# Kernel tuning notes

Hardware: AMD Instinct MI355X
Metric: run time of the kernel (lower is better)

Reference implementation:

```python
import jax, jax.numpy as jnp
import numpy as np

B, S, D, H = 4, 1024, 1024, 16
HD = D // H


def setup_inputs() -> dict:
    key = jax.random.key(0)
    ks = jax.random.split(key, 12)
    s = 1.0 / np.sqrt(D)
    inp = {
        'q': jax.random.normal(ks[0], (B, S, D), jnp.float32),
        'k': jax.random.normal(ks[1], (B, S, D), jnp.float32),
        'v': jax.random.normal(ks[2], (B, S, D), jnp.float32),
        'mask': jnp.broadcast_to(jnp.tril(jnp.ones((S, S), jnp.int32)), (B, S, S)),
        'Wq': jax.random.uniform(ks[3], (D, D), jnp.float32, -s, s),
        'bq': jax.random.uniform(ks[4], (D,), jnp.float32, -s, s),
        'Wk': jax.random.uniform(ks[5], (D, D), jnp.float32, -s, s),
        'bk': jax.random.uniform(ks[6], (D,), jnp.float32, -s, s),
        'Wv': jax.random.uniform(ks[7], (D, D), jnp.float32, -s, s),
        'bv': jax.random.uniform(ks[8], (D,), jnp.float32, -s, s),
        'Wo': jax.random.uniform(ks[9], (D, D), jnp.float32, -s, s),
        'bo': jax.random.uniform(ks[10], (D,), jnp.float32, -s, s),
    }
    return inp


def _split_heads(x):
    # [B,S,D] -> [B,H,S,HD]
    b, s, d = x.shape
    return x.reshape(b, s, H, HD).transpose(0, 2, 1, 3)


def reference(q, k, v, mask, Wq, bq, Wk, bk, Wv, bv, Wo, bo):
    # Linear projections (torch Linear: x @ W.T + b) followed by relu
    qh = jax.nn.relu(q @ Wq.T + bq)
    kh = jax.nn.relu(k @ Wk.T + bk)
    vh = jax.nn.relu(v @ Wv.T + bv)
    qh, kh, vh = _split_heads(qh), _split_heads(kh), _split_heads(vh)
    scores = jnp.einsum('bhqd,bhkd->bhqk', qh, kh) / jnp.sqrt(jnp.float32(HD))
    scores = jnp.where(mask[:, None, :, :] == 0, jnp.float32(-1e9), scores)
    attn = jax.nn.softmax(scores, axis=-1)
    y = jnp.einsum('bhqk,bhkd->bhqd', attn, vh)
    y = y.transpose(0, 2, 1, 3).reshape(B, S, D)  # merge heads
    return jax.nn.relu(y @ Wo.T + bo)
```

## Files before the change

### kernel.cpp

```cpp
#include <hip/hip_runtime.h>


using f16    = _Float16;
using f16x4  = __attribute__((ext_vector_type(4))) _Float16;
using f16x8  = __attribute__((ext_vector_type(8))) _Float16;
using f32x4  = __attribute__((ext_vector_type(4))) float;
using f32x16 = __attribute__((ext_vector_type(16))) float;

static constexpr int S = 1024, Dm = 1024, NH = 16, HD = 64;

#if __has_builtin(__builtin_amdgcn_mfma_f32_32x32x16_f16)
#define USE_G32 1
#define MFMA32(ACC, A_, B_) \
    (ACC) = __builtin_amdgcn_mfma_f32_32x32x16_f16((A_), (B_), (ACC), 0, 0, 0)
#else
#define USE_G32 0
#endif

#if __has_builtin(__builtin_amdgcn_mfma_f32_16x16x32_f16) && \
    __has_builtin(__builtin_amdgcn_mfma_f32_16x16x16f16)
#define USE_A16 1
#define MFMA16K32(ACC, A_, B_) \
    (ACC) = __builtin_amdgcn_mfma_f32_16x16x32_f16((A_), (B_), (ACC), 0, 0, 0)
#define MFMA16(ACC, A_, B_) \
    (ACC) = __builtin_amdgcn_mfma_f32_16x16x16f16((A_), (B_), (ACC), 0, 0, 0)
#else
#define USE_A16 0
#endif

#define LO4(v) __builtin_shufflevector((v), (v), 0, 1, 2, 3)
#define HI4(v) __builtin_shufflevector((v), (v), 4, 5, 6, 7)

__device__ __forceinline__ f16x4 cvt4(float4 a) {
    f16x4 r; r[0] = (f16)a.x; r[1] = (f16)a.y; r[2] = (f16)a.z; r[3] = (f16)a.w;
    return r;
}

__device__ __forceinline__ int pcol64(int k) {
#if USE_A16
    return ((k >> 3) & 3) * 16 + ((k >> 5) << 3) + (k & 7);
#else
    return ((k >> 2) & 3) * 16 + ((k >> 4) << 2) + (k & 3);
#endif
}

__device__ __forceinline__ int swz(int row, int col) {
    return (col & ~31) | ((((col >> 3) ^ (row >> 1)) & 3) << 3) | (col & 7);
}

__device__ __forceinline__ void store_out(void* out, int mode, int m, int n, float v) {
    if (mode == 2) {
        ((float*)out)[(size_t)m * Dm + n] = v;
    } else {
        const int b_ = m >> 10, s_ = m & 1023, h_ = n >> 6, hd_ = n & 63;
        const size_t idx = (mode == 0)
            ? (((size_t)(b_ * NH + h_) * S + s_) * HD + pcol64(hd_))
            : (((size_t)(b_ * NH + h_) * HD + hd_) * S + s_);
        ((f16*)out)[idx] = (f16)v;
    }
}

#if __has_builtin(__builtin_amdgcn_global_load_lds)
#define HAS_GLL 1
#else
#define HAS_GLL 0
#endif

__device__ __forceinline__ void gll16(const f16* g, f16* l) {
#if HAS_GLL
    __builtin_amdgcn_global_load_lds(
        (const __attribute__((address_space(1))) void*)g,
        (__attribute__((address_space(3))) void*)l, 16, 0, 0);
#else
    *(uint4*)l = *(const uint4*)g;
#endif
}

__global__ __launch_bounds__(256)
void cvt_w(const float* __restrict__ s0, const float* __restrict__ s1,
           const float* __restrict__ s2, f16* __restrict__ dst)
{
    const int z = blockIdx.y;
    const float* src = (z == 0) ? s0 : (z == 1) ? s1 : s2;
    const int e = blockIdx.x * 256 + threadIdx.x;
    const int n = e >> 8;
    const int k = (e & 255) * 4;
    const float4 v = *(const float4*)(src + (size_t)n * Dm + k);
    *(f16x4*)(dst + (size_t)z * Dm * Dm + (size_t)n * Dm + swz(n, k)) = cvt4(v);
}

template <int ADMA>
__device__ __forceinline__ void gemm_core(const void* __restrict__ A,
                                          const f16* __restrict__ Wf,
                                          const float* __restrict__ bias,
                                          void* __restrict__ out, int mode)
{
    const int tid = threadIdx.x;
    const int bm = blockIdx.x, bn = blockIdx.y;
#if USE_G32
    __shared__ alignas(16) f16 As[3][128][32];
    __shared__ alignas(16) f16 Ws[3][128][32];

    const int lane = tid & 63, wave = tid >> 6;
    const int l31 = lane & 31, kh = lane >> 5;
    const int wm = wave & 1, wn = wave >> 1;

    const int drow = wave * 16 + (lane >> 2);
    const int dcol = (lane & 3) * 8;
    const f16* Wsrc = Wf + (size_t)(bn * 128 + drow) * Dm + dcol;
    const f16* Asrc = (const f16*)A + (size_t)(bm * 128 + drow) * Dm + dcol;

    auto dma = [&](int k0, int buf) {
        gll16(Wsrc + k0, &Ws[buf][drow][dcol]);
        gll16(Wsrc + k0 + (size_t)64 * Dm, &Ws[buf][64 + drow][dcol]);
        if (ADMA) {
            gll16(Asrc + k0, &As[buf][drow][dcol]);
            gll16(Asrc + k0 + (size_t)64 * Dm, &As[buf][64 + drow][dcol]);
        }
    };

    const int ar = tid >> 1, ah = tid & 1;
    const float* Af = (const float*)A + (size_t)(bm * 128 + ar) * Dm + ah * 16;

    auto prefA = [&](int k0, float4 (&pa)[4]) {
#pragma unroll
        for (int j = 0; j < 4; ++j) pa[j] = *(const float4*)(Af + k0 + j * 4);
    };
    auto stageA = [&](int buf, const float4 (&pa)[4]) {
#pragma unroll
        for (int j2 = 0; j2 < 2; ++j2) {
            f16x8 v;
            const float4 a0 = pa[j2 * 2], a1 = pa[j2 * 2 + 1];
            v[0] = (f16)a0.x; v[1] = (f16)a0.y; v[2] = (f16)a0.z; v[3] = (f16)a0.w;
            v[4] = (f16)a1.x; v[5] = (f16)a1.y; v[6] = (f16)a1.z; v[7] = (f16)a1.w;
            const int phys = ((ah * 2 + j2) ^ ((ar >> 1) & 3)) & 3;
            *(f16x8*)&As[buf][ar][phys * 8] = v;
        }
    };

    f32x16 acc[2][2] = {};

    auto kslice = [&](int buf, int s) {
        const int sl = s * 2 + kh;
        const int rA0 = wm * 64 + l31,  rA1 = wm * 64 + 32 + l31;
        const int rB0 = wn * 64 + l31,  rB1 = wn * 64 + 32 + l31;
        const f16x8 af0 = *(const f16x8*)&As[buf][rA0][((sl ^ ((rA0 >> 1) & 3)) & 3) * 8];
        const f16x8 af1 = *(const f16x8*)&As[buf][rA1][((sl ^ ((rA1 >> 1) & 3)) & 3) * 8];
        const f16x8 bf0 = *(const f16x8*)&Ws[buf][rB0][((sl ^ ((rB0 >> 1) & 3)) & 3) * 8];
        const f16x8 bf1 = *(const f16x8*)&Ws[buf][rB1][((sl ^ ((rB1 >> 1) & 3)) & 3) * 8];
        MFMA32(acc[0][0], af0, bf0);
        MFMA32(acc[0][1], af0, bf1);
        MFMA32(acc[1][0], af1, bf0);
        MFMA32(acc[1][1], af1, bf1);
    };

    constexpr int NIT = Dm / 32;
    float4 paA[4], paB[4];

    if (!ADMA) prefA(0, paA);
    dma(0, 0);
    if (!ADMA) prefA(32, paB);
    dma(32, 1);
    if (!ADMA) stageA(0, paA);

    auto iter = [&](int t, float4 (&pnew)[4], const float4 (&pold)[4]) {
        if (t < NIT - 1) {
            if (ADMA) asm volatile("s_waitcnt vmcnt(4)" ::: "memory");
            else      asm volatile("s_waitcnt vmcnt(6)" ::: "memory");
        } else {
            asm volatile("s_waitcnt vmcnt(0)" ::: "memory");
        }
        asm volatile("s_waitcnt lgkmcnt(0)" ::: "memory");
        __builtin_amdgcn_s_barrier();
        __builtin_amdgcn_sched_barrier(0);
        const int cb = t % 3;
        if (t + 2 < NIT) {
            if (!ADMA) prefA((t + 2) * 32, pnew);
            dma((t + 2) * 32, (t + 2) % 3);
        }
        kslice(cb, 0);
        if (!ADMA && t + 1 < NIT) stageA((t + 1) % 3, pold);
        kslice(cb, 1);
    };

    for (int t = 0; t < NIT; t += 2) {
        iter(t, paA, paB);
        iter(t + 1, paB, paA);
    }

#pragma unroll
    for (int g2 = 0; g2 < 2; ++g2) {
        const int col = bn * 128 + wn * 64 + g2 * 32 + l31;
        const float bb = bias[col];
#pragma unroll
        for (int g = 0; g < 2; ++g)
#pragma unroll
            for (int blk = 0; blk < 4; ++blk) {
                const int row0 = bm * 128 + wm * 64 + g * 32 + 8 * blk + 4 * kh;
                if (mode == 1) {
                    const int b_ = row0 >> 10, s_ = row0 & 1023;
                    const int h_ = col >> 6, hd_ = col & 63;
                    f16x4 vv;
#pragma unroll
                    for (int r = 0; r < 4; ++r)
                        vv[r] = (f16)fmaxf(acc[g][g2][blk * 4 + r] + bb, 0.0f);
                    *(f16x4*)&((f16*)out)[((size_t)(b_ * NH + h_) * HD + hd_) * S + s_] = vv;
                } else {
#pragma unroll
                    for (int r = 0; r < 4; ++r)
                        store_out(out, mode, row0 + r, col,
                                  fmaxf(acc[g][g2][blk * 4 + r] + bb, 0.0f));
                }
            }
    }
#else
    for (int i = tid; i < 128 * 128; i += 256) {
        const int m = bm * 128 + (i >> 7);
        const int n = bn * 128 + (i & 127);
        float acc = 0.0f;
        for (int k2 = 0; k2 < Dm; ++k2) {
            const float a = ADMA ? (float)((const f16*)A)[(size_t)m * Dm + swz(m, k2)]
                                 : ((const float*)A)[(size_t)m * Dm + k2];
            acc = fmaf(a, (float)Wf[(size_t)n * Dm + swz(n, k2)], acc);
        }
        store_out(out, mode, m, n, fmaxf(acc + bias[n], 0.0f));
    }
#endif
}

__global__ __launch_bounds__(256, 3)
void gemm_qkv(const float* __restrict__ q, const float* __restrict__ k,
              const float* __restrict__ v, const f16* __restrict__ wqkv,
              const float* __restrict__ bq, const float* __restrict__ bk,
              const float* __restrict__ bv,
              f16* __restrict__ qh, f16* __restrict__ kh, f16* __restrict__ vt)
{
    const int z = blockIdx.z;
    const float* A = (z == 0) ? q : (z == 1) ? k : v;
    const float* B = (z == 0) ? bq : (z == 1) ? bk : bv;
    f16* O = (z == 0) ? qh : (z == 1) ? kh : vt;
    gemm_core<0>(A, wqkv + (size_t)z * Dm * Dm, B, O, (z == 2) ? 1 : 0);
}

__global__ __launch_bounds__(256, 3)
void gemm_out(const f16* __restrict__ y, const f16* __restrict__ wo,
              const float* __restrict__ bo, float* __restrict__ out)
{
    gemm_core<1>(y, wo, bo, out, 2);
}

__global__ __launch_bounds__(256)
void attn_fwd(const f16* __restrict__ qh, const f16* __restrict__ kh,
              const f16* __restrict__ vt, f16* __restrict__ y)
{
    const int bz = blockIdx.x;
    const int qt = bz & 15;
    const int h  = (bz >> 4) & 15;
    const int b  = bz >> 8;
    const size_t head = (size_t)(b * NH + h) * S * HD;

#if USE_A16
    __shared__ alignas(16) f16 Ks[2][64][72];
    __shared__ alignas(16) f16 Vs[2][64][72];

    const int tid  = threadIdx.x;
    const int wave = tid >> 6;
    const int lane = tid & 63;
    const int l15  = lane & 15;
    const int quad = lane >> 4;
    const int sr   = tid >> 2;
    const int sc   = (tid & 3) * 16;

    const f16* Qrow = qh + head + (size_t)(qt * 64 + wave * 16 + l15) * HD;
    const f16* Kp   = kh + head;
    const f16* Vp   = vt + head;

    f16x8 aq[2];
    {
        const uint4 q0 = *(const uint4*)(Qrow + quad * 16);
        const uint4 q1 = *(const uint4*)(Qrow + quad * 16 + 8);
        aq[0] = *(f16x8*)&q0;
        aq[1] = *(f16x8*)&q1;
    }

    const int qg = qt * 64 + wave * 16 + l15;
    float m_i = -1e30f, l_i = 0.0f;
    f32x4 acc_o[4] = {};

    uint4 pk[2], pv[2];
    auto pref = [&](int kt) {
        const f16* Kr = Kp + (size_t)(kt * 64 + sr) * HD + sc;
        pk[0] = *(const uint4*)Kr;
        pk[1] = *(const uint4*)(Kr + 8);
        const f16* Vr = Vp + (size_t)sr * S + kt * 64 + sc;
        pv[0] = *(const uint4*)Vr;
        pv[1] = *(const uint4*)(Vr + 8);
    };

    pref(0);
    for (int kt = 0; kt <= qt; ++kt) {
        const int cur = kt & 1;
        *(uint4*)&Ks[cur][sr][sc]     = pk[0];
        *(uint4*)&Ks[cur][sr][sc + 8] = pk[1];
        {
            const int sb = (sc >> 4) * 4;
            *(f16x4*)&Vs[cur][sr][0 * 16 + sb] = *(f16x4*)((f16*)&pv[0]);
            *(f16x4*)&Vs[cur][sr][1 * 16 + sb] = *(f16x4*)((f16*)&pv[0] + 4);
            *(f16x4*)&Vs[cur][sr][2 * 16 + sb] = *(f16x4*)((f16*)&pv[1]);
            *(f16x4*)&Vs[cur][sr][3 * 16 + sb] = *(f16x4*)((f16*)&pv[1] + 4);
        }
        __syncthreads();
        if (kt < qt) pref(kt + 1);

        f32x4 accs[4] = {};
#pragma unroll
        for (int t = 0; t < 4; ++t) {
            const f16x8 k8a = *(const f16x8*)&Ks[cur][t * 16 + l15][quad * 16];
            const f16x8 k8b = *(const f16x8*)&Ks[cur][t * 16 + l15][quad * 16 + 8];
            MFMA16K32(accs[t], k8a, aq[0]);
            MFMA16K32(accs[t], k8b, aq[1]);
        }

        const int key0 = kt * 64 + quad * 4;
#pragma unroll
        for (int t = 0; t < 4; ++t)
#pragma unroll
            for (int r = 0; r < 4; ++r) {
                float sv = accs[t][r] * 0.125f;
                if (key0 + t * 16 + r > qg) sv = -1e9f;
                accs[t][r] = sv;
            }

        float mx = accs[0][0];
#pragma unroll
        for (int t = 0; t < 4; ++t)
#pragma unroll
            for (int r = 0; r < 4; ++r) mx = fmaxf(mx, accs[t][r]);
        mx = fmaxf(mx, __shfl_xor(mx, 16, 64));
        mx = fmaxf(mx, __shfl_xor(mx, 32, 64));
        const float mnew = fmaxf(m_i, mx);
        float sm = 0.0f;
#pragma unroll
        for (int t = 0; t < 4; ++t)
#pragma unroll
            for (int r = 0; r < 4; ++r) {
                const float e = __expf(accs[t][r] - mnew);
                accs[t][r] = e;
                sm += e;
            }
        sm += __shfl_xor(sm, 16, 64);
        sm += __shfl_xor(sm, 32, 64);
        const float alpha = __expf(m_i - mnew);
        l_i = l_i * alpha + sm;
        m_i = mnew;

        f16x4 ap[4];
#pragma unroll
        for (int c = 0; c < 4; ++c) {
            f16x4 v;
#pragma unroll
            for (int j = 0; j < 4; ++j) v[j] = (f16)accs[c][j];
            ap[c] = v;
        }

        float ar[4];
#pragma unroll
        for (int r = 0; r < 4; ++r) ar[r] = __shfl(alpha, quad * 4 + r, 64);
#pragma unroll
        for (int t2 = 0; t2 < 4; ++t2)
#pragma unroll
            for (int r = 0; r < 4; ++r) acc_o[t2][r] *= ar[r];
#pragma unroll
        for (int t2 = 0; t2 < 4; ++t2) {
            const f16x8 v8a = *(const f16x8*)&Vs[cur][t2 * 16 + l15][quad * 16];
            const f16x8 v8b = *(const f16x8*)&Vs[cur][t2 * 16 + l15][quad * 16 + 8];
            MFMA16(acc_o[t2], ap[0], LO4(v8a));
            MFMA16(acc_o[t2], ap[1], HI4(v8a));
            MFMA16(acc_o[t2], ap[2], LO4(v8b));
            MFMA16(acc_o[t2], ap[3], HI4(v8b));
        }
    }

    float lr[4];
#pragma unroll
    for (int r = 0; r < 4; ++r) lr[r] = __shfl(l_i, quad * 4 + r, 64);
#pragma unroll
    for (int t2 = 0; t2 < 4; ++t2)
#pragma unroll
        for (int r = 0; r < 4; ++r) {
            const int srow = qt * 64 + wave * 16 + quad * 4 + r;
            const int dcol = h * 64 + t2 * 16 + l15;
            y[((size_t)b * S + srow) * Dm + swz(srow, dcol)] =
                (f16)(acc_o[t2][r] / lr[r]);
        }
#else
    const int tid = threadIdx.x;
    if (tid < 64) {
        const int q = qt * 64 + tid;
        const f16* Qr = qh + head + (size_t)q * HD;
        float qv[64];
        for (int d = 0; d < 64; ++d) qv[d] = (float)Qr[pcol64(d)];
        float mx = -1e30f;
        for (int key = 0; key <= q; ++key) {
            const f16* Kr = kh + head + (size_t)key * HD;
            float s = 0.0f;
            for (int d = 0; d < 64; ++d) s = fmaf(qv[d], (float)Kr[pcol64(d)], s);
            mx = fmaxf(mx, s * 0.125f);
        }
        float o[64];
        for (int d = 0; d < 64; ++d) o[d] = 0.0f;
        float l = 0.0f;
        for (int key = 0; key <= q; ++key) {
            const f16* Kr = kh + head + (size_t)key * HD;
            float s = 0.0f;
            for (int d = 0; d < 64; ++d) s = fmaf(qv[d], (float)Kr[pcol64(d)], s);
            const float p = __expf(s * 0.125f - mx);
            l += p;
            for (int d = 0; d < 64; ++d)
                o[d] = fmaf(p, (float)vt[head + (size_t)d * S + key], o[d]);
        }
        for (int d = 0; d < 64; ++d)
            y[((size_t)b * S + q) * Dm + swz(q, h * 64 + d)] = (f16)(o[d] / l);
    }
#endif
}

extern "C" void kernel_launch(void* const* d_in, const int* in_sizes, int n_in,
                              void* d_out, int out_size, void* d_ws, size_t ws_size,
                              hipStream_t stream)
{
    f16* ws = (f16*)d_ws;
    const size_t SEG = (size_t)4 * 1024 * 1024;
    f16* qh   = ws;
    f16* kh   = ws + SEG;
    f16* vt   = ws + 2 * SEG;
    f16* wqkv = ws + 3 * SEG;
    f16* y    = ws + 3 * SEG;
    f16* wo   = ws;

    cvt_w<<<dim3(1024, 3), 256, 0, stream>>>(
        (const float*)d_in[4], (const float*)d_in[6], (const float*)d_in[8], wqkv);
    gemm_qkv<<<dim3(32, 8, 3), 256, 0, stream>>>(
        (const float*)d_in[0], (const float*)d_in[1], (const float*)d_in[2],
        wqkv,
        (const float*)d_in[5], (const float*)d_in[7], (const float*)d_in[9],
        qh, kh, vt);
    attn_fwd<<<dim3(4 * NH * (S / 64)), 256, 0, stream>>>(qh, kh, vt, y);
    cvt_w<<<dim3(1024, 1), 256, 0, stream>>>(
        (const float*)d_in[10], nullptr, nullptr, wo);
    gemm_out<<<dim3(32, 8), 256, 0, stream>>>(
        y, wo, (const float*)d_in[11], (float*)d_out);
}
```

Baseline: 259.2 us.

## Use 512-thread blocks with 8 waves per 128x128 GEMM tile

Raises the projection GEMM blocks from 4 to 8 waves. Each wave now computes a 32x64 sub-tile with two accumulators instead of 64x64 with four, and loads and DMA work are split across more threads with fewer per-thread loads and adjusted vmcnt waits. The aim is more latency hiding and less register pressure per wave. The cost is less reuse of A fragments per wave and more LDS reads per MFMA, and the launch-bound occupancy hints change.

After: 252.6 us. -2.5%, faster.

```diff
diff --git a/kernel.cpp b/kernel.cpp
--- a/kernel.cpp
+++ b/kernel.cpp
@@ -103,59 +103,48 @@
 
     const int lane = tid & 63, wave = tid >> 6;
     const int l31 = lane & 31, kh = lane >> 5;
-    const int wm = wave & 1, wn = wave >> 1;
-
-    const int drow = wave * 16 + (lane >> 2);
-    const int dcol = (lane & 3) * 8;
+    const int wm = wave & 3, wn = wave >> 2;
+
+    const int drow = tid >> 2;
+    const int dcol = (tid & 3) * 8;
     const f16* Wsrc = Wf + (size_t)(bn * 128 + drow) * Dm + dcol;
     const f16* Asrc = (const f16*)A + (size_t)(bm * 128 + drow) * Dm + dcol;
 
     auto dma = [&](int k0, int buf) {
         gll16(Wsrc + k0, &Ws[buf][drow][dcol]);
-        gll16(Wsrc + k0 + (size_t)64 * Dm, &Ws[buf][64 + drow][dcol]);
-        if (ADMA) {
-            gll16(Asrc + k0, &As[buf][drow][dcol]);
-            gll16(Asrc + k0 + (size_t)64 * Dm, &As[buf][64 + drow][dcol]);
-        }
-    };
-
-    const int ar = tid >> 1, ah = tid & 1;
-    const float* Af = (const float*)A + (size_t)(bm * 128 + ar) * Dm + ah * 16;
-
-    auto prefA = [&](int k0, float4 (&pa)[4]) {
-#pragma unroll
-        for (int j = 0; j < 4; ++j) pa[j] = *(const float4*)(Af + k0 + j * 4);
-    };
-    auto stageA = [&](int buf, const float4 (&pa)[4]) {
-#pragma unroll
-        for (int j2 = 0; j2 < 2; ++j2) {
-            f16x8 v;
-            const float4 a0 = pa[j2 * 2], a1 = pa[j2 * 2 + 1];
-            v[0] = (f16)a0.x; v[1] = (f16)a0.y; v[2] = (f16)a0.z; v[3] = (f16)a0.w;
-            v[4] = (f16)a1.x; v[5] = (f16)a1.y; v[6] = (f16)a1.z; v[7] = (f16)a1.w;
-            const int phys = ((ah * 2 + j2) ^ ((ar >> 1) & 3)) & 3;
-            *(f16x8*)&As[buf][ar][phys * 8] = v;
-        }
-    };
-
-    f32x16 acc[2][2] = {};
+        if (ADMA) gll16(Asrc + k0, &As[buf][drow][dcol]);
+    };
+
+    const int ar = tid >> 2, aslot = tid & 3;
+    const float* Af = (const float*)A + (size_t)(bm * 128 + ar) * Dm + aslot * 8;
+
+    auto prefA = [&](int k0, float4 (&pa)[2]) {
+        pa[0] = *(const float4*)(Af + k0);
+        pa[1] = *(const float4*)(Af + k0 + 4);
+    };
+    auto stageA = [&](int buf, const float4 (&pa)[2]) {
+        f16x8 v;
+        v[0] = (f16)pa[0].x; v[1] = (f16)pa[0].y; v[2] = (f16)pa[0].z; v[3] = (f16)pa[0].w;
+        v[4] = (f16)pa[1].x; v[5] = (f16)pa[1].y; v[6] = (f16)pa[1].z; v[7] = (f16)pa[1].w;
+        const int phys = (aslot ^ ((ar >> 1) & 3)) & 3;
+        *(f16x8*)&As[buf][ar][phys * 8] = v;
+    };
+
+    f32x16 acc[2] = {};
 
     auto kslice = [&](int buf, int s) {
         const int sl = s * 2 + kh;
-        const int rA0 = wm * 64 + l31,  rA1 = wm * 64 + 32 + l31;
-        const int rB0 = wn * 64 + l31,  rB1 = wn * 64 + 32 + l31;
-        const f16x8 af0 = *(const f16x8*)&As[buf][rA0][((sl ^ ((rA0 >> 1) & 3)) & 3) * 8];
-        const f16x8 af1 = *(const f16x8*)&As[buf][rA1][((sl ^ ((rA1 >> 1) & 3)) & 3) * 8];
+        const int rA = wm * 32 + l31;
+        const int rB0 = wn * 64 + l31, rB1 = wn * 64 + 32 + l31;
+        const f16x8 af  = *(const f16x8*)&As[buf][rA][((sl ^ ((rA >> 1) & 3)) & 3) * 8];
         const f16x8 bf0 = *(const f16x8*)&Ws[buf][rB0][((sl ^ ((rB0 >> 1) & 3)) & 3) * 8];
         const f16x8 bf1 = *(const f16x8*)&Ws[buf][rB1][((sl ^ ((rB1 >> 1) & 3)) & 3) * 8];
-        MFMA32(acc[0][0], af0, bf0);
-        MFMA32(acc[0][1], af0, bf1);
-        MFMA32(acc[1][0], af1, bf0);
-        MFMA32(acc[1][1], af1, bf1);
+        MFMA32(acc[0], af, bf0);
+        MFMA32(acc[1], af, bf1);
     };
 
     constexpr int NIT = Dm / 32;
-    float4 paA[4], paB[4];
+    float4 paA[2], paB[2];
 
     if (!ADMA) prefA(0, paA);
     dma(0, 0);
@@ -163,10 +152,10 @@
     dma(32, 1);
     if (!ADMA) stageA(0, paA);
 
-    auto iter = [&](int t, float4 (&pnew)[4], const float4 (&pold)[4]) {
+    auto iter = [&](int t, float4 (&pnew)[2], const float4 (&pold)[2]) {
         if (t < NIT - 1) {
-            if (ADMA) asm volatile("s_waitcnt vmcnt(4)" ::: "memory");
-            else      asm volatile("s_waitcnt vmcnt(6)" ::: "memory");
+            if (ADMA) asm volatile("s_waitcnt vmcnt(2)" ::: "memory");
+            else      asm volatile("s_waitcnt vmcnt(3)" ::: "memory");
         } else {
             asm volatile("s_waitcnt vmcnt(0)" ::: "memory");
         }
@@ -189,32 +178,30 @@
     }
 
 #pragma unroll
-    for (int g2 = 0; g2 < 2; ++g2) {
-        const int col = bn * 128 + wn * 64 + g2 * 32 + l31;
+    for (int j = 0; j < 2; ++j) {
+        const int col = bn * 128 + wn * 64 + j * 32 + l31;
         const float bb = bias[col];
 #pragma unroll
-        for (int g = 0; g < 2; ++g)
-#pragma unroll
-            for (int blk = 0; blk < 4; ++blk) {
-                const int row0 = bm * 128 + wm * 64 + g * 32 + 8 * blk + 4 * kh;
-                if (mode == 1) {
-                    const int b_ = row0 >> 10, s_ = row0 & 1023;
-                    const int h_ = col >> 6, hd_ = col & 63;
-                    f16x4 vv;
-#pragma unroll
-                    for (int r = 0; r < 4; ++r)
-                        vv[r] = (f16)fmaxf(acc[g][g2][blk * 4 + r] + bb, 0.0f);
-                    *(f16x4*)&((f16*)out)[((size_t)(b_ * NH + h_) * HD + hd_) * S + s_] = vv;
-                } else {
-#pragma unroll
-                    for (int r = 0; r < 4; ++r)
-                        store_out(out, mode, row0 + r, col,
-                                  fmaxf(acc[g][g2][blk * 4 + r] + bb, 0.0f));
-                }
+        for (int blk = 0; blk < 4; ++blk) {
+            const int row0 = bm * 128 + wm * 32 + 8 * blk + 4 * kh;
+            if (mode == 1) {
+                const int b_ = row0 >> 10, s_ = row0 & 1023;
+                const int h_ = col >> 6, hd_ = col & 63;
+                f16x4 vv;
+#pragma unroll
+                for (int r = 0; r < 4; ++r)
+                    vv[r] = (f16)fmaxf(acc[j][blk * 4 + r] + bb, 0.0f);
+                *(f16x4*)&((f16*)out)[((size_t)(b_ * NH + h_) * HD + hd_) * S + s_] = vv;
+            } else {
+#pragma unroll
+                for (int r = 0; r < 4; ++r)
+                    store_out(out, mode, row0 + r, col,
+                              fmaxf(acc[j][blk * 4 + r] + bb, 0.0f));
             }
-    }
-#else
-    for (int i = tid; i < 128 * 128; i += 256) {
+        }
+    }
+#else
+    for (int i = tid; i < 128 * 128; i += 512) {
         const int m = bm * 128 + (i >> 7);
         const int n = bn * 128 + (i & 127);
         float acc = 0.0f;
@@ -228,7 +215,7 @@
 #endif
 }
 
-__global__ __launch_bounds__(256, 3)
+__global__ __launch_bounds__(512, 6)
 void gemm_qkv(const float* __restrict__ q, const float* __restrict__ k,
               const float* __restrict__ v, const f16* __restrict__ wqkv,
               const float* __restrict__ bq, const float* __restrict__ bk,
@@ -242,7 +229,7 @@
     gemm_core<0>(A, wqkv + (size_t)z * Dm * Dm, B, O, (z == 2) ? 1 : 0);
 }
 
-__global__ __launch_bounds__(256, 3)
+__global__ __launch_bounds__(512, 2)
 void gemm_out(const f16* __restrict__ y, const f16* __restrict__ wo,
               const float* __restrict__ bo, float* __restrict__ out)
 {
@@ -440,7 +427,7 @@
 
     cvt_w<<<dim3(1024, 3), 256, 0, stream>>>(
         (const float*)d_in[4], (const float*)d_in[6], (const float*)d_in[8], wqkv);
-    gemm_qkv<<<dim3(32, 8, 3), 256, 0, stream>>>(
+    gemm_qkv<<<dim3(32, 8, 3), 512, 0, stream>>>(
         (const float*)d_in[0], (const float*)d_in[1], (const float*)d_in[2],
         wqkv,
         (const float*)d_in[5], (const float*)d_in[7], (const float*)d_in[9],
@@ -448,6 +435,6 @@
     attn_fwd<<<dim3(4 * NH * (S / 64)), 256, 0, stream>>>(qh, kh, vt, y);
     cvt_w<<<dim3(1024, 1), 256, 0, stream>>>(
         (const float*)d_in[10], nullptr, nullptr, wo);
-    gemm_out<<<dim3(32, 8), 256, 0, stream>>>(
+    gemm_out<<<dim3(32, 8), 512, 0, stream>>>(
         y, wo, (const float*)d_in[11], (float*)d_out);
 }
```
